# Kernel tuning notes

Measured on AMD Instinct MI355X. Metric: run time of the kernel, lower is better.

## Reference

```python
import jax, jax.numpy as jnp
import numpy as np

B, N, X_DIM, Y_DIM = 2048, 64, 2, 1
Z_DIM, R_DIM, H = 64, 128, 128
STEPS = 20
SIGMA_SQ = 1.0


def setup_inputs() -> dict:
    key = jax.random.key(0)
    ks = jax.random.split(key, 16)

    def w(k, shape):
        return jax.random.normal(k, shape, dtype=jnp.float32) / np.float32(np.sqrt(shape[0]))

    return {
        "x_ctx": jax.random.normal(ks[0], (B, N, X_DIM), jnp.float32),
        "y_ctx": jax.random.normal(ks[1], (B, N, Y_DIM), jnp.float32),
        "mask": jnp.ones((B, N, 1), jnp.float32),
        "z0": jax.random.normal(ks[2], (B, Z_DIM), jnp.float32),
        "noises": jax.random.normal(ks[3], (STEPS, B, Z_DIM), jnp.float32),
        "We1": w(ks[4], (X_DIM + Y_DIM, H)), "be1": jnp.zeros((H,), jnp.float32),
        "We2": w(ks[5], (H, H)), "be2": jnp.zeros((H,), jnp.float32),
        "We3": w(ks[6], (H, R_DIM)), "be3": jnp.zeros((R_DIM,), jnp.float32),
        "Wd1": w(ks[7], (Z_DIM + X_DIM, H)), "bd1": jnp.zeros((H,), jnp.float32),
        "Wd2": w(ks[8], (H, H)), "bd2": jnp.zeros((H,), jnp.float32),
        "Wd3": w(ks[9], (H, Y_DIM)), "bd3": jnp.zeros((Y_DIM,), jnp.float32),
        "Wf1": w(ks[10], (Z_DIM + R_DIM + 1, H)), "bf1": jnp.zeros((H,), jnp.float32),
        "Wf2": w(ks[11], (H, H)), "bf2": jnp.zeros((H,), jnp.float32),
        "Wf3": w(ks[12], (H, Z_DIM)), "bf3": jnp.zeros((Z_DIM,), jnp.float32),
        "steps": STEPS,
    }


def reference(x_ctx, y_ctx, mask, z0, noises,
              We1, be1, We2, be2, We3, be3,
              Wd1, bd1, Wd2, bd2, Wd3, bd3,
              Wf1, bf1, Wf2, bf2, Wf3, bf3,
              steps):
    silu = jax.nn.silu
    n_ctx = x_ctx.shape[1]

    # encoder: masked mean-pool set MLP -> r [B, R_DIM]
    h = silu(jnp.concatenate([x_ctx, y_ctx], axis=-1) @ We1 + be1)
    h = silu(h @ We2 + be2)
    h = h @ We3 + be3  # [B, N, R_DIM]
    r = jnp.sum(h * mask, axis=1) / jnp.clip(jnp.sum(mask, axis=1), 1e-6)

    def decoder(z):
        zb = jnp.broadcast_to(z[:, None, :], (z.shape[0], n_ctx, z.shape[1]))
        d = silu(jnp.concatenate([zb, x_ctx], axis=-1) @ Wd1 + bd1)
        d = silu(d @ Wd2 + bd2)
        return d @ Wd3 + bd3  # [B, N, Y_DIM]

    def energy_sum(z, t):
        # U_t(z) = u_prior + t * u_lik  (== (1-t)*u_prior + t*(u_prior + u_lik))
        u_prior = 0.5 * jnp.sum(z * z, axis=1)
        sq_err = (y_ctx - decoder(z)) ** 2 * mask
        u_lik = 0.5 * jnp.sum(sq_err, axis=(1, 2)) / SIGMA_SQ
        return jnp.sum(u_prior + t * u_lik)

    def drift(z, t_col):
        f = silu(jnp.concatenate([z, r, t_col], axis=-1) @ Wf1 + bf1)
        f = silu(f @ Wf2 + bf2)
        return f @ Wf3 + bf3

    dt = 1.0 / steps
    diff_coef = float(np.sqrt(2.0 * dt))

    def step(z, xs):
        t, noise = xs
        g = jnp.clip(jax.grad(energy_sum)(z, t), -100.0, 100.0)
        t_col = jnp.ones((z.shape[0], 1), z.dtype) * t
        b = drift(z, t_col)
        z = z + (-g + b) * dt + diff_coef * noise
        return z, None

    ts = jnp.arange(steps, dtype=jnp.float32) * dt
    z_final, _ = jax.lax.scan(jax.checkpoint(step), z0, (ts, noises))
    return z_final
```

## Files before the change

### kernel.cpp

```cpp
#include <hip/hip_runtime.h>
#include <math.h>


#define B_TOT 2048
#define NPT   64
#define ZD    64
#define HD    128

typedef short bh8 __attribute__((ext_vector_type(8)));
typedef float fx4 __attribute__((ext_vector_type(4)));

__device__ __forceinline__ float sigf(float x) {
  return __builtin_amdgcn_rcpf(1.0f + __expf(-x));
}
__device__ __forceinline__ unsigned int bfb(float x) {
  unsigned int u = __float_as_uint(x);
  u += 0x7FFFu + ((u >> 16) & 1u);
  return u >> 16;
}
__device__ __forceinline__ unsigned int cvtpk(float a, float b) {
  unsigned int r;
  asm("v_cvt_pk_bf16_f32 %0, %1, %2" : "=v"(r) : "v"(a), "v"(b));
  return r;
}
__device__ __forceinline__ float wsum64(float v) {
  #pragma unroll
  for (int d = 1; d < 64; d <<= 1) v += __shfl_xor(v, d, 64);
  return v;
}
__device__ __forceinline__ void wave_sync() {
  __builtin_amdgcn_wave_barrier();
  __builtin_amdgcn_s_waitcnt(0xC07F);
  __builtin_amdgcn_wave_barrier();
}

__global__ __launch_bounds__(256)
void prep_kernel(const float* __restrict__ Wd2, const float* __restrict__ We2,
                 const float* __restrict__ We3, const float* __restrict__ Wd1,
                 ushort* __restrict__ ws) {
  const int id = blockIdx.x * 256 + threadIdx.x;
  if (id < 65536) {
    const int arr = id >> 14;
    const int e = id & 16383;
    const int j = e & 7, L = (e >> 3) & 63, nt = (e >> 9) & 7, kc = e >> 12;
    const int kk = kc * 32 + (L >> 4) * 8 + j, nn = nt * 16 + (L & 15);
    float v;
    if      (arr == 0) v = Wd2[kk * HD + nn];
    else if (arr == 1) v = Wd2[nn * HD + kk];
    else if (arr == 2) v = We2[kk * HD + nn];
    else               v = We3[kk * HD + nn];
    ws[id] = (ushort)bfb(v);
  } else {
    const int e = id - 65536;
    const int h = e >> 6, jj = e & 63;
    ((float*)(ws + 65536))[e] = Wd1[jj * HD + h];
  }
}

__global__ __launch_bounds__(256, 4)
void metanets_kernel(
    const float* __restrict__ x_ctx, const float* __restrict__ y_ctx,
    const float* __restrict__ mask,  const float* __restrict__ z0,
    const float* __restrict__ noises,
    const float* __restrict__ We1, const float* __restrict__ be1,
    const float* __restrict__ be2, const float* __restrict__ be3,
    const float* __restrict__ Wd1, const float* __restrict__ bd1,
    const float* __restrict__ bd2, const float* __restrict__ Wd3,
    const float* __restrict__ bd3,
    const float* __restrict__ Wf1, const float* __restrict__ bf1,
    const float* __restrict__ Wf2, const float* __restrict__ bf2,
    const float* __restrict__ Wf3, const float* __restrict__ bf3,
    const ushort* __restrict__ wsfrag,
    float* __restrict__ out, int steps, float dt, float dco)
{
  __shared__ unsigned int h1f[4096];
  __shared__ float zsh[64];
  __shared__ float zw1[128];
  __shared__ float rsh[128];
  __shared__ float dsumP[512];
  __shared__ float dsumC[128];
  __shared__ float f1sh[128];
  __shared__ float f2sh[128];
  __shared__ float bgz[128];
  __shared__ float rw1sh[128];
  __shared__ float wt1sh[128];
  __shared__ float ysh[64], mksh[64];
  __shared__ float bd2sh[128], wd3sh[128], wx0sh[128], wx1sh[128];

  const int tid = threadIdx.x;
  const int lane = tid & 63;
  const int w = __builtin_amdgcn_readfirstlane(tid >> 6);
  const int b = blockIdx.x;
  const int rr = lane & 15, qq = lane >> 4;

  const bh8* Wd2f  = (const bh8*)(wsfrag);
  const bh8* Wd2Tf = (const bh8*)(wsfrag + 16384);
  const bh8* We2f  = (const bh8*)(wsfrag + 32768);
  const bh8* We3f  = (const bh8*)(wsfrag + 49152);
  const float* Wd1T = (const float*)(wsfrag + 65536);

  const float x0v = x_ctx[(b*NPT + lane)*2 + 0];
  const float x1v = x_ctx[(b*NPT + lane)*2 + 1];
  const float yv  = y_ctx[b*NPT + lane];
  const float mkv = mask[b*NPT + lane];
  const float inv_msum = 1.0f / fmaxf(wsum64(mkv), 1e-6f);
  const float bd3v = bd3[0];

  float x0q[4], x1q[4];
  #pragma unroll
  for (int g = 0; g < 4; ++g) {
    const int src = (w << 4) | (qq << 2) | g;
    x0q[g] = __shfl(x0v, src, 64);
    x1q[g] = __shfl(x1v, src, 64);
  }

  if (tid < 64) {
    zsh[tid]  = z0[b*ZD + tid];
    ysh[tid]  = yv;
    mksh[tid] = mkv;
  }
  if (tid < 128) {
    bd2sh[tid] = bd2[tid];
    wd3sh[tid] = Wd3[tid];
    wx0sh[tid] = Wd1[64*HD + tid];
    wx1sh[tid] = Wd1[65*HD + tid];
    f1sh[tid]  = be2[tid];
    f2sh[tid]  = be3[tid];
    wt1sh[tid] = Wf1[192*HD + tid];
  }
  __syncthreads();

  #pragma unroll
  for (int quad = 0; quad < 4; ++quad) {
    unsigned int pw[4];
    #pragma unroll
    for (int jj = 0; jj < 8; jj += 2) {
      const int k = 32*w + 8*quad + jj;
      const float sA = be1[k]   + x0v*We1[k]   + x1v*We1[HD+k]   + yv*We1[2*HD+k];
      const float sB = be1[k+1] + x0v*We1[k+1] + x1v*We1[HD+k+1] + yv*We1[2*HD+k+1];
      pw[jj>>1] = cvtpk(sA*sigf(sA), sB*sigf(sB));
    }
    uint4 v4; v4.x = pw[0]; v4.y = pw[1]; v4.z = pw[2]; v4.w = pw[3];
    ((uint4*)h1f)[(w*4 + (lane>>4))*64 + quad*16 + (lane&15)] = v4;
  }
  __syncthreads();

  {
    bh8 af[4];
    #pragma unroll
    for (int kc = 0; kc < 4; ++kc)
      af[kc] = ((const bh8*)h1f)[(kc*4 + w)*64 + lane];
    #pragma unroll 1
    for (int np = 0; np < 4; ++np) {
      const int nt0 = 2*np, nt1 = 2*np + 1;
      const bh8 a0 = We2f[(0*8+nt0)*64 + lane];
      const bh8 a1 = We2f[(1*8+nt0)*64 + lane];
      const bh8 a2 = We2f[(2*8+nt0)*64 + lane];
      const bh8 a3 = We2f[(3*8+nt0)*64 + lane];
      const bh8 c0 = We2f[(0*8+nt1)*64 + lane];
      const bh8 c1 = We2f[(1*8+nt1)*64 + lane];
      const bh8 c2 = We2f[(2*8+nt1)*64 + lane];
      const bh8 c3 = We2f[(3*8+nt1)*64 + lane];
      const float bv0 = f1sh[nt0*16 + rr], bv1 = f1sh[nt1*16 + rr];
      fx4 acc0 = (fx4){bv0, bv0, bv0, bv0};
      fx4 acc1 = (fx4){bv1, bv1, bv1, bv1};
      acc0 = __builtin_amdgcn_mfma_f32_16x16x32_bf16(af[0], a0, acc0, 0,0,0);
      acc1 = __builtin_amdgcn_mfma_f32_16x16x32_bf16(af[0], c0, acc1, 0,0,0);
      acc0 = __builtin_amdgcn_mfma_f32_16x16x32_bf16(af[1], a1, acc0, 0,0,0);
      acc1 = __builtin_amdgcn_mfma_f32_16x16x32_bf16(af[1], c1, acc1, 0,0,0);
      acc0 = __builtin_amdgcn_mfma_f32_16x16x32_bf16(af[2], a2, acc0, 0,0,0);
      acc1 = __builtin_amdgcn_mfma_f32_16x16x32_bf16(af[2], c2, acc1, 0,0,0);
      acc0 = __builtin_amdgcn_mfma_f32_16x16x32_bf16(af[3], a3, acc0, 0,0,0);
      acc1 = __builtin_amdgcn_mfma_f32_16x16x32_bf16(af[3], c3, acc1, 0,0,0);
      #pragma unroll
      for (int pi = 0; pi < 2; ++pi) {
        const int nt = pi ? nt1 : nt0;
        const fx4 acc = pi ? acc1 : acc0;
        #pragma unroll
        for (int g = 0; g < 4; ++g) {
          const float s2 = acc[g];
          const float tf = s2 * sigf(s2);
          const float pf = __shfl_xor(tf, 1, 64);
          if ((rr & 1) == 0) {
            const int unit = ((nt>>1)*4 + w)*64 + (2*(nt&1) + (rr>>3))*16 + 4*qq + g;
            h1f[unit*4 + ((rr&7)>>1)] = cvtpk(tf, pf);
          }
        }
      }
    }
  }
  wave_sync();

  {
    float mkq0, mkq1, mkq2, mkq3;
    {
      const int s0 = (w << 4) | (qq << 2);
      mkq0 = mksh[s0+0]; mkq1 = mksh[s0+1]; mkq2 = mksh[s0+2]; mkq3 = mksh[s0+3];
    }
    bh8 tf4[4];
    #pragma unroll
    for (int kc = 0; kc < 4; ++kc)
      tf4[kc] = ((const bh8*)h1f)[(kc*4 + w)*64 + lane];
    #pragma unroll 1
    for (int np = 0; np < 4; ++np) {
      const int nt0 = 2*np, nt1 = 2*np + 1;
      const bh8 a0 = We3f[(0*8+nt0)*64 + lane];
      const bh8 a1 = We3f[(1*8+nt0)*64 + lane];
      const bh8 a2 = We3f[(2*8+nt0)*64 + lane];
      const bh8 a3 = We3f[(3*8+nt0)*64 + lane];
      const bh8 c0 = We3f[(0*8+nt1)*64 + lane];
      const bh8 c1 = We3f[(1*8+nt1)*64 + lane];
      const bh8 c2 = We3f[(2*8+nt1)*64 + lane];
      const bh8 c3 = We3f[(3*8+nt1)*64 + lane];
      const float bv0 = f2sh[nt0*16 + rr], bv1 = f2sh[nt1*16 + rr];
      fx4 acc0 = (fx4){bv0, bv0, bv0, bv0};
      fx4 acc1 = (fx4){bv1, bv1, bv1, bv1};
      acc0 = __builtin_amdgcn_mfma_f32_16x16x32_bf16(tf4[0], a0, acc0, 0,0,0);
      acc1 = __builtin_amdgcn_mfma_f32_16x16x32_bf16(tf4[0], c0, acc1, 0,0,0);
      acc0 = __builtin_amdgcn_mfma_f32_16x16x32_bf16(tf4[1], a1, acc0, 0,0,0);
      acc1 = __builtin_amdgcn_mfma_f32_16x16x32_bf16(tf4[1], c1, acc1, 0,0,0);
      acc0 = __builtin_amdgcn_mfma_f32_16x16x32_bf16(tf4[2], a2, acc0, 0,0,0);
      acc1 = __builtin_amdgcn_mfma_f32_16x16x32_bf16(tf4[2], c2, acc1, 0,0,0);
      acc0 = __builtin_amdgcn_mfma_f32_16x16x32_bf16(tf4[3], a3, acc0, 0,0,0);
      acc1 = __builtin_amdgcn_mfma_f32_16x16x32_bf16(tf4[3], c3, acc1, 0,0,0);
      #pragma unroll
      for (int pi = 0; pi < 2; ++pi) {
        const int nt = pi ? nt1 : nt0;
        const fx4 acc = pi ? acc1 : acc0;
        float pv = mkq0*acc[0] + mkq1*acc[1] + mkq2*acc[2] + mkq3*acc[3];
        pv += __shfl_xor(pv, 16, 64);
        pv += __shfl_xor(pv, 32, 64);
        if (lane < 16) dsumP[w*128 + nt*16 + lane] = pv;
      }
    }
  }
  __syncthreads();
  if (tid < 128)
    rsh[tid] = (dsumP[tid] + dsumP[128+tid] + dsumP[256+tid] + dsumP[384+tid]) * inv_msum;
  __syncthreads();

  if (tid < 128) {
    float p0 = bf1[tid], p1 = 0.f, p2 = 0.f, p3 = 0.f;
    #pragma unroll 4
    for (int j = 0; j < 128; j += 4) {
      p0 = fmaf(rsh[j+0], Wf1[(64+j+0)*HD + tid], p0);
      p1 = fmaf(rsh[j+1], Wf1[(64+j+1)*HD + tid], p1);
      p2 = fmaf(rsh[j+2], Wf1[(64+j+2)*HD + tid], p2);
      p3 = fmaf(rsh[j+3], Wf1[(64+j+3)*HD + tid], p3);
    }
    rw1sh[tid] = (p0+p1) + (p2+p3);
  }
  __syncthreads();

  for (int st = 0; st < steps; ++st) {
    const float t = (float)st * dt;
    const int zi = tid & 63;

    const float noise_v = noises[(size_t)st * (B_TOT * ZD) + b * ZD + zi];
    const float zold_r  = zsh[zi];

    if (tid < 128) {
      float p0 = bd1[tid], p1 = 0.f, p2 = 0.f, p3 = 0.f;
      #pragma unroll 4
      for (int j = 0; j < 64; j += 4) {
        p0 = fmaf(zsh[j+0], Wd1[(j+0)*HD + tid], p0);
        p1 = fmaf(zsh[j+1], Wd1[(j+1)*HD + tid], p1);
        p2 = fmaf(zsh[j+2], Wd1[(j+2)*HD + tid], p2);
        p3 = fmaf(zsh[j+3], Wd1[(j+3)*HD + tid], p3);
      }
      zw1[tid] = (p0+p1) + (p2+p3);
    } else {
      const int o = tid - 128;
      float p0 = fmaf(t, wt1sh[o], rw1sh[o]);
      float p1 = 0.f, p2 = 0.f, p3 = 0.f;
      #pragma unroll 4
      for (int j = 0; j < 64; j += 4) {
        p0 = fmaf(zsh[j+0], Wf1[(j+0)*HD + o], p0);
        p1 = fmaf(zsh[j+1], Wf1[(j+1)*HD + o], p1);
        p2 = fmaf(zsh[j+2], Wf1[(j+2)*HD + o], p2);
        p3 = fmaf(zsh[j+3], Wf1[(j+3)*HD + o], p3);
      }
      const float a = (p0+p1) + (p2+p3);
      f1sh[o] = a * sigf(a);
    }
    __syncthreads();

    #pragma unroll
    for (int quad = 0; quad < 4; ++quad) {
      unsigned int pw[4];
      #pragma unroll
      for (int jj = 0; jj < 8; jj += 2) {
        const int k = 32*w + 8*quad + jj;
        const float sA = zw1[k]   + x0v*wx0sh[k]   + x1v*wx1sh[k];
        const float sB = zw1[k+1] + x0v*wx0sh[k+1] + x1v*wx1sh[k+1];
        pw[jj>>1] = cvtpk(sA*sigf(sA), sB*sigf(sB));
      }
      uint4 v4; v4.x = pw[0]; v4.y = pw[1]; v4.z = pw[2]; v4.w = pw[3];
      ((uint4*)h1f)[(w*4 + (lane>>4))*64 + quad*16 + (lane&15)] = v4;
    }
    __syncthreads();

    float ebw[4];
    {
      bh8 af[4];
      #pragma unroll
      for (int kc = 0; kc < 4; ++kc)
        af[kc] = ((const bh8*)h1f)[(kc*4 + w)*64 + lane];
      float da[4] = {0.f, 0.f, 0.f, 0.f};
      #pragma unroll 1
      for (int np = 0; np < 4; ++np) {
        const int nt0 = 2*np, nt1 = 2*np + 1;
        const bh8 a0 = Wd2f[(0*8+nt0)*64 + lane];
        const bh8 a1 = Wd2f[(1*8+nt0)*64 + lane];
        const bh8 a2 = Wd2f[(2*8+nt0)*64 + lane];
        const bh8 a3 = Wd2f[(3*8+nt0)*64 + lane];
        const bh8 c0 = Wd2f[(0*8+nt1)*64 + lane];
        const bh8 c1 = Wd2f[(1*8+nt1)*64 + lane];
        const bh8 c2 = Wd2f[(2*8+nt1)*64 + lane];
        const bh8 c3 = Wd2f[(3*8+nt1)*64 + lane];
        const float bv0 = bd2sh[nt0*16 + rr], bv1 = bd2sh[nt1*16 + rr];
        fx4 acc0 = (fx4){bv0, bv0, bv0, bv0};
        fx4 acc1 = (fx4){bv1, bv1, bv1, bv1};
        acc0 = __builtin_amdgcn_mfma_f32_16x16x32_bf16(af[0], a0, acc0, 0,0,0);
        acc1 = __builtin_amdgcn_mfma_f32_16x16x32_bf16(af[0], c0, acc1, 0,0,0);
        acc0 = __builtin_amdgcn_mfma_f32_16x16x32_bf16(af[1], a1, acc0, 0,0,0);
        acc1 = __builtin_amdgcn_mfma_f32_16x16x32_bf16(af[1], c1, acc1, 0,0,0);
        acc0 = __builtin_amdgcn_mfma_f32_16x16x32_bf16(af[2], a2, acc0, 0,0,0);
        acc1 = __builtin_amdgcn_mfma_f32_16x16x32_bf16(af[2], c2, acc1, 0,0,0);
        acc0 = __builtin_amdgcn_mfma_f32_16x16x32_bf16(af[3], a3, acc0, 0,0,0);
        acc1 = __builtin_amdgcn_mfma_f32_16x16x32_bf16(af[3], c3, acc1, 0,0,0);
        #pragma unroll
        for (int pi = 0; pi < 2; ++pi) {
          const int nt = pi ? nt1 : nt0;
          const fx4 acc = pi ? acc1 : acc0;
          const float w3 = wd3sh[nt*16 + rr];
          #pragma unroll
          for (int g = 0; g < 4; ++g) {
            const float s2 = acc[g];
            const float sg = sigf(s2);
            da[g] = fmaf(s2*sg, w3, da[g]);
            const float tf = w3 * (sg * fmaf(s2, 1.0f - sg, 1.0f));
            const float pf = __shfl_xor(tf, 1, 64);
            if ((rr & 1) == 0) {
              const int unit = ((nt>>1)*4 + w)*64 + (2*(nt&1) + (rr>>3))*16 + 4*qq + g;
              h1f[unit*4 + ((rr&7)>>1)] = cvtpk(tf, pf);
            }
          }
        }
      }
      const int s0 = (w << 4) | (qq << 2);
      #pragma unroll
      for (int g = 0; g < 4; ++g) {
        float v = da[g];
        v += __shfl_xor(v, 1, 64);
        v += __shfl_xor(v, 2, 64);
        v += __shfl_xor(v, 4, 64);
        v += __shfl_xor(v, 8, 64);
        ebw[g] = t * mksh[s0+g] * (v + bd3v - ysh[s0+g]);
      }
    }
    wave_sync();

    {
      bh8 tf4[4];
      #pragma unroll
      for (int kc = 0; kc < 4; ++kc)
        tf4[kc] = ((const bh8*)h1f)[(kc*4 + w)*64 + lane];
      #pragma unroll 1
      for (int np = 0; np < 4; ++np) {
        const int nt0 = 2*np, nt1 = 2*np + 1;
        const bh8 a0 = Wd2Tf[(0*8+nt0)*64 + lane];
        const bh8 a1 = Wd2Tf[(1*8+nt0)*64 + lane];
        const bh8 a2 = Wd2Tf[(2*8+nt0)*64 + lane];
        const bh8 a3 = Wd2Tf[(3*8+nt0)*64 + lane];
        const bh8 c0 = Wd2Tf[(0*8+nt1)*64 + lane];
        const bh8 c1 = Wd2Tf[(1*8+nt1)*64 + lane];
        const bh8 c2 = Wd2Tf[(2*8+nt1)*64 + lane];
        const bh8 c3 = Wd2Tf[(3*8+nt1)*64 + lane];
        fx4 u0 = (fx4){0.f, 0.f, 0.f, 0.f};
        fx4 u1 = (fx4){0.f, 0.f, 0.f, 0.f};
        u0 = __builtin_amdgcn_mfma_f32_16x16x32_bf16(tf4[0], a0, u0, 0,0,0);
        u1 = __builtin_amdgcn_mfma_f32_16x16x32_bf16(tf4[0], c0, u1, 0,0,0);
        u0 = __builtin_amdgcn_mfma_f32_16x16x32_bf16(tf4[1], a1, u0, 0,0,0);
        u1 = __builtin_amdgcn_mfma_f32_16x16x32_bf16(tf4[1], c1, u1, 0,0,0);
        u0 = __builtin_amdgcn_mfma_f32_16x16x32_bf16(tf4[2], a2, u0, 0,0,0);
        u1 = __builtin_amdgcn_mfma_f32_16x16x32_bf16(tf4[2], c2, u1, 0,0,0);
        u0 = __builtin_amdgcn_mfma_f32_16x16x32_bf16(tf4[3], a3, u0, 0,0,0);
        u1 = __builtin_amdgcn_mfma_f32_16x16x32_bf16(tf4[3], c3, u1, 0,0,0);
        #pragma unroll
        for (int pi = 0; pi < 2; ++pi) {
          const int nt = pi ? nt1 : nt0;
          const fx4 u = pi ? u1 : u0;
          const float zv = zw1[nt*16 + rr];
          const float wa = wx0sh[nt*16 + rr];
          const float wb = wx1sh[nt*16 + rr];
          float snt = 0.f;
          #pragma unroll
          for (int g = 0; g < 4; ++g) {
            const float s1 = zv + x0q[g]*wa + x1q[g]*wb;
            const float sg = sigf(s1);
            snt += ebw[g] * (sg * fmaf(s1, 1.0f - sg, 1.0f)) * u[g];
          }
          snt += __shfl_xor(snt, 16, 64);
          snt += __shfl_xor(snt, 32, 64);
          if (lane < 16) dsumP[w*128 + nt*16 + lane] = snt;
        }
      }
    }
    __syncthreads();

    if (tid < 128) {
      dsumC[tid] = dsumP[tid] + dsumP[128+tid] + dsumP[256+tid] + dsumP[384+tid];
      float p0 = 0.f, p1 = 0.f, p2 = 0.f, p3 = 0.f;
      #pragma unroll 4
      for (int j = 64; j < 128; j += 4) {
        p0 = fmaf(f1sh[j+0], Wf2[(j+0)*HD + tid], p0);
        p1 = fmaf(f1sh[j+1], Wf2[(j+1)*HD + tid], p1);
        p2 = fmaf(f1sh[j+2], Wf2[(j+2)*HD + tid], p2);
        p3 = fmaf(f1sh[j+3], Wf2[(j+3)*HD + tid], p3);
      }
      rsh[tid] = (p0+p1) + (p2+p3);
    } else {
      const int o = tid - 128;
      float p0 = bf2[o], p1 = 0.f, p2 = 0.f, p3 = 0.f;
      #pragma unroll 4
      for (int j = 0; j < 64; j += 4) {
        p0 = fmaf(f1sh[j+0], Wf2[(j+0)*HD + o], p0);
        p1 = fmaf(f1sh[j+1], Wf2[(j+1)*HD + o], p1);
        p2 = fmaf(f1sh[j+2], Wf2[(j+2)*HD + o], p2);
        p3 = fmaf(f1sh[j+3], Wf2[(j+3)*HD + o], p3);
      }
      zw1[o] = (p0+p1) + (p2+p3);
    }
    __syncthreads();

    if (tid < 128) {
      const int j = tid & 63, h0 = (tid >> 6) * 64;
      float p0 = 0.f, p1 = 0.f, p2 = 0.f, p3 = 0.f;
      #pragma unroll 4
      for (int h = 0; h < 64; h += 4) {
        p0 = fmaf(dsumC[h0+h+0], Wd1T[(h0+h+0)*64 + j], p0);
        p1 = fmaf(dsumC[h0+h+1], Wd1T[(h0+h+1)*64 + j], p1);
        p2 = fmaf(dsumC[h0+h+2], Wd1T[(h0+h+2)*64 + j], p2);
        p3 = fmaf(dsumC[h0+h+3], Wd1T[(h0+h+3)*64 + j], p3);
      }
      dsumP[tid] = (p0+p1) + (p2+p3);
    } else {
      const int o = tid - 128;
      const float a = rsh[o] + zw1[o];
      f2sh[o] = a * sigf(a);
      wave_sync();
      const int j = o & 63, h0 = (o >> 6) * 64;
      float p0 = (h0 == 0) ? bf3[j] : 0.f;
      float p1 = 0.f, p2 = 0.f, p3 = 0.f;
      #pragma unroll 4
      for (int h = 0; h < 64; h += 4) {
        p0 = fmaf(f2sh[h0+h+0], Wf3[(h0+h+0)*ZD + j], p0);
        p1 = fmaf(f2sh[h0+h+1], Wf3[(h0+h+1)*ZD + j], p1);
        p2 = fmaf(f2sh[h0+h+2], Wf3[(h0+h+2)*ZD + j], p2);
        p3 = fmaf(f2sh[h0+h+3], Wf3[(h0+h+3)*ZD + j], p3);
      }
      bgz[o] = (p0+p1) + (p2+p3);
    }
    __syncthreads();

    {
      const float bdrift = bgz[zi] + bgz[64 + zi];
      const float gzv    = dsumP[zi] + dsumP[64 + zi];
      float g = zold_r + gzv;
      g = fminf(fmaxf(g, -100.0f), 100.0f);
      zsh[zi] = zold_r + (bdrift - g) * dt + dco * noise_v;
    }
    wave_sync();
  }

  if (tid < 64) out[b * ZD + tid] = zsh[tid];
}

extern "C" void kernel_launch(void* const* d_in, const int* in_sizes, int n_in,
                              void* d_out, int out_size, void* d_ws, size_t ws_size,
                              hipStream_t stream) {
  const float* x_ctx  = (const float*)d_in[0];
  const float* y_ctx  = (const float*)d_in[1];
  const float* mask   = (const float*)d_in[2];
  const float* z0     = (const float*)d_in[3];
  const float* noises = (const float*)d_in[4];
  const float* We1 = (const float*)d_in[5];  const float* be1 = (const float*)d_in[6];
  const float* We2 = (const float*)d_in[7];  const float* be2 = (const float*)d_in[8];
  const float* We3 = (const float*)d_in[9];  const float* be3 = (const float*)d_in[10];
  const float* Wd1 = (const float*)d_in[11]; const float* bd1 = (const float*)d_in[12];
  const float* Wd2 = (const float*)d_in[13]; const float* bd2 = (const float*)d_in[14];
  const float* Wd3 = (const float*)d_in[15]; const float* bd3 = (const float*)d_in[16];
  const float* Wf1 = (const float*)d_in[17]; const float* bf1 = (const float*)d_in[18];
  const float* Wf2 = (const float*)d_in[19]; const float* bf2 = (const float*)d_in[20];
  const float* Wf3 = (const float*)d_in[21]; const float* bf3 = (const float*)d_in[22];

  const int steps = in_sizes[4] / (B_TOT * ZD);
  const float dt  = 1.0f / (float)steps;
  const float dco = (float)sqrt(2.0 / (double)steps);

  ushort* wsu = (ushort*)d_ws;

  hipLaunchKernelGGL(prep_kernel, dim3(288), dim3(256), 0, stream,
                     Wd2, We2, We3, Wd1, wsu);
  hipLaunchKernelGGL(metanets_kernel, dim3(B_TOT), dim3(256), 0, stream,
      x_ctx, y_ctx, mask, z0, noises,
      We1, be1, be2, be3,
      Wd1, bd1, bd2, Wd3, bd3,
      Wf1, bf1, Wf2, bf2, Wf3, bf3,
      wsu, (float*)d_out, steps, dt, dco);
}
```

Before: 838.0 us.

## Use packed fp32 FMA with pair-interleaved weight layouts for small GEMVs

Prep kernel now writes Wd1, Wf1, Wf2, Wf3 and transposed Wd1 into pair-interleaved fp32 layouts so each thread loads a float2 and issues a packed FMA. The first-layer GEMV is remapped so every wave computes half decoder and half drift outputs, and its block barrier becomes a wave barrier. This aims to halve FMA instruction count and widen loads in the per-step small matvecs. The wave-local sync depends on each wave consuming only the zw1/f1sh entries it wrote, and the interleaved layout adds workspace and prep cost.

```diff
diff --git a/kernel.cpp b/kernel.cpp
--- a/kernel.cpp
+++ b/kernel.cpp
@@ -9,6 +9,7 @@
 
 typedef short bh8 __attribute__((ext_vector_type(8)));
 typedef float fx4 __attribute__((ext_vector_type(4)));
+typedef float fx2 __attribute__((ext_vector_type(2)));
 
 __device__ __forceinline__ float sigf(float x) {
   return __builtin_amdgcn_rcpf(1.0f + __expf(-x));
@@ -23,6 +24,9 @@
   asm("v_cvt_pk_bf16_f32 %0, %1, %2" : "=v"(r) : "v"(a), "v"(b));
   return r;
 }
+__device__ __forceinline__ fx2 pkfma(fx2 a, fx2 b, fx2 c) {
+  return __builtin_elementwise_fma(a, b, c);
+}
 __device__ __forceinline__ float wsum64(float v) {
   #pragma unroll
   for (int d = 1; d < 64; d <<= 1) v += __shfl_xor(v, d, 64);
@@ -37,7 +41,8 @@
 __global__ __launch_bounds__(256)
 void prep_kernel(const float* __restrict__ Wd2, const float* __restrict__ We2,
                  const float* __restrict__ We3, const float* __restrict__ Wd1,
-                 ushort* __restrict__ ws) {
+                 const float* __restrict__ Wf1, const float* __restrict__ Wf2,
+                 const float* __restrict__ Wf3, ushort* __restrict__ ws) {
   const int id = blockIdx.x * 256 + threadIdx.x;
   if (id < 65536) {
     const int arr = id >> 14;
@@ -50,10 +55,26 @@
     else if (arr == 2) v = We2[kk * HD + nn];
     else               v = We3[kk * HD + nn];
     ws[id] = (ushort)bfb(v);
+  } else if (id < 73728) {
+    const int e = id - 65536;
+    const int j2 = e >> 8, o = (e >> 1) & 127, lohi = e & 1;
+    ((float*)(ws + 65536))[e] = Wd1[(2*j2 + lohi)*HD + o];
+  } else if (id < 81920) {
+    const int e = id - 73728;
+    const int j2 = e >> 8, o = (e >> 1) & 127, lohi = e & 1;
+    ((float*)(ws + 81920))[e] = Wf1[(2*j2 + lohi)*HD + o];
+  } else if (id < 98304) {
+    const int e = id - 81920;
+    const int j2 = e >> 8, o = (e >> 1) & 127, lohi = e & 1;
+    ((float*)(ws + 98304))[e] = Wf2[(2*j2 + lohi)*HD + o];
+  } else if (id < 106496) {
+    const int e = id - 98304;
+    const int h2 = e >> 7, j = (e >> 1) & 63, lohi = e & 1;
+    ((float*)(ws + 131072))[e] = Wf3[(2*h2 + lohi)*ZD + j];
   } else {
-    const int e = id - 65536;
-    const int h = e >> 6, jj = e & 63;
-    ((float*)(ws + 65536))[e] = Wd1[jj * HD + h];
+    const int e = id - 106496;
+    const int h2 = e >> 7, j = (e >> 1) & 63, lohi = e & 1;
+    ((float*)(ws + 147456))[e] = Wd1[j*HD + (2*h2 + lohi)];
   }
 }
 
@@ -74,13 +95,13 @@
     float* __restrict__ out, int steps, float dt, float dco)
 {
   __shared__ unsigned int h1f[4096];
-  __shared__ float zsh[64];
-  __shared__ float zw1[128];
+  __shared__ __align__(8) float zsh[64];
+  __shared__ __align__(8) float zw1[128];
   __shared__ float rsh[128];
+  __shared__ __align__(8) float dsumC[128];
   __shared__ float dsumP[512];
-  __shared__ float dsumC[128];
-  __shared__ float f1sh[128];
-  __shared__ float f2sh[128];
+  __shared__ __align__(8) float f1sh[128];
+  __shared__ __align__(8) float f2sh[128];
   __shared__ float bgz[128];
   __shared__ float rw1sh[128];
   __shared__ float wt1sh[128];
@@ -97,7 +118,11 @@
   const bh8* Wd2Tf = (const bh8*)(wsfrag + 16384);
   const bh8* We2f  = (const bh8*)(wsfrag + 32768);
   const bh8* We3f  = (const bh8*)(wsfrag + 49152);
-  const float* Wd1T = (const float*)(wsfrag + 65536);
+  const fx2* Wd1P  = (const fx2*)(wsfrag + 65536);
+  const fx2* Wf1zP = (const fx2*)(wsfrag + 81920);
+  const fx2* Wf2P  = (const fx2*)(wsfrag + 98304);
+  const fx2* Wf3P  = (const fx2*)(wsfrag + 131072);
+  const fx2* Wd1TP = (const fx2*)(wsfrag + 147456);
 
   const float x0v = x_ctx[(b*NPT + lane)*2 + 0];
   const float x1v = x_ctx[(b*NPT + lane)*2 + 1];
@@ -259,31 +284,28 @@
     const float noise_v = noises[(size_t)st * (B_TOT * ZD) + b * ZD + zi];
     const float zold_r  = zsh[zi];
 
-    if (tid < 128) {
-      float p0 = bd1[tid], p1 = 0.f, p2 = 0.f, p3 = 0.f;
+    {
+      const int oA = 32*w + (lane & 31);
+      const bool isz = (lane < 32);
+      const fx2* Wp = (isz ? Wd1P : Wf1zP) + oA;
+      fx2 a0 = (fx2){ isz ? bd1[oA] : fmaf(t, wt1sh[oA], rw1sh[oA]), 0.f };
+      fx2 a1 = (fx2){0.f, 0.f}, a2 = a1, a3 = a1;
       #pragma unroll 4
-      for (int j = 0; j < 64; j += 4) {
-        p0 = fmaf(zsh[j+0], Wd1[(j+0)*HD + tid], p0);
-        p1 = fmaf(zsh[j+1], Wd1[(j+1)*HD + tid], p1);
-        p2 = fmaf(zsh[j+2], Wd1[(j+2)*HD + tid], p2);
-        p3 = fmaf(zsh[j+3], Wd1[(j+3)*HD + tid], p3);
-      }
-      zw1[tid] = (p0+p1) + (p2+p3);
-    } else {
-      const int o = tid - 128;
-      float p0 = fmaf(t, wt1sh[o], rw1sh[o]);
-      float p1 = 0.f, p2 = 0.f, p3 = 0.f;
-      #pragma unroll 4
-      for (int j = 0; j < 64; j += 4) {
-        p0 = fmaf(zsh[j+0], Wf1[(j+0)*HD + o], p0);
-        p1 = fmaf(zsh[j+1], Wf1[(j+1)*HD + o], p1);
-        p2 = fmaf(zsh[j+2], Wf1[(j+2)*HD + o], p2);
-        p3 = fmaf(zsh[j+3], Wf1[(j+3)*HD + o], p3);
-      }
-      const float a = (p0+p1) + (p2+p3);
-      f1sh[o] = a * sigf(a);
-    }
-    __syncthreads();
+      for (int j2 = 0; j2 < 32; j2 += 4) {
+        const fx2 z0 = *(const fx2*)&zsh[2*(j2+0)];
+        const fx2 z1 = *(const fx2*)&zsh[2*(j2+1)];
+        const fx2 z2 = *(const fx2*)&zsh[2*(j2+2)];
+        const fx2 z3 = *(const fx2*)&zsh[2*(j2+3)];
+        a0 = pkfma(z0, Wp[(j2+0)*128], a0);
+        a1 = pkfma(z1, Wp[(j2+1)*128], a1);
+        a2 = pkfma(z2, Wp[(j2+2)*128], a2);
+        a3 = pkfma(z3, Wp[(j2+3)*128], a3);
+      }
+      const float a = ((a0.x+a0.y)+(a1.x+a1.y)) + ((a2.x+a2.y)+(a3.x+a3.y));
+      if (isz) zw1[oA] = a;
+      else     f1sh[oA] = a * sigf(a);
+    }
+    wave_sync();
 
     #pragma unroll
     for (int quad = 0; quad < 4; ++quad) {
@@ -411,56 +433,76 @@
 
     if (tid < 128) {
       dsumC[tid] = dsumP[tid] + dsumP[128+tid] + dsumP[256+tid] + dsumP[384+tid];
-      float p0 = 0.f, p1 = 0.f, p2 = 0.f, p3 = 0.f;
+      const fx2* Wp = Wf2P + tid;
+      fx2 a0 = (fx2){0.f, 0.f}, a1 = a0, a2 = a0, a3 = a0;
       #pragma unroll 4
-      for (int j = 64; j < 128; j += 4) {
-        p0 = fmaf(f1sh[j+0], Wf2[(j+0)*HD + tid], p0);
-        p1 = fmaf(f1sh[j+1], Wf2[(j+1)*HD + tid], p1);
-        p2 = fmaf(f1sh[j+2], Wf2[(j+2)*HD + tid], p2);
-        p3 = fmaf(f1sh[j+3], Wf2[(j+3)*HD + tid], p3);
-      }
-      rsh[tid] = (p0+p1) + (p2+p3);
+      for (int j2 = 32; j2 < 64; j2 += 4) {
+        const fx2 f0 = *(const fx2*)&f1sh[2*(j2+0)];
+        const fx2 f1v = *(const fx2*)&f1sh[2*(j2+1)];
+        const fx2 f2v = *(const fx2*)&f1sh[2*(j2+2)];
+        const fx2 f3v = *(const fx2*)&f1sh[2*(j2+3)];
+        a0 = pkfma(f0,  Wp[(j2+0)*128], a0);
+        a1 = pkfma(f1v, Wp[(j2+1)*128], a1);
+        a2 = pkfma(f2v, Wp[(j2+2)*128], a2);
+        a3 = pkfma(f3v, Wp[(j2+3)*128], a3);
+      }
+      rsh[tid] = ((a0.x+a0.y)+(a1.x+a1.y)) + ((a2.x+a2.y)+(a3.x+a3.y));
     } else {
       const int o = tid - 128;
-      float p0 = bf2[o], p1 = 0.f, p2 = 0.f, p3 = 0.f;
+      const fx2* Wp = Wf2P + o;
+      fx2 a0 = (fx2){bf2[o], 0.f}, a1 = (fx2){0.f,0.f}, a2 = a1, a3 = a1;
       #pragma unroll 4
-      for (int j = 0; j < 64; j += 4) {
-        p0 = fmaf(f1sh[j+0], Wf2[(j+0)*HD + o], p0);
-        p1 = fmaf(f1sh[j+1], Wf2[(j+1)*HD + o], p1);
-        p2 = fmaf(f1sh[j+2], Wf2[(j+2)*HD + o], p2);
-        p3 = fmaf(f1sh[j+3], Wf2[(j+3)*HD + o], p3);
-      }
-      zw1[o] = (p0+p1) + (p2+p3);
+      for (int j2 = 0; j2 < 32; j2 += 4) {
+        const fx2 f0 = *(const fx2*)&f1sh[2*(j2+0)];
+        const fx2 f1v = *(const fx2*)&f1sh[2*(j2+1)];
+        const fx2 f2v = *(const fx2*)&f1sh[2*(j2+2)];
+        const fx2 f3v = *(const fx2*)&f1sh[2*(j2+3)];
+        a0 = pkfma(f0,  Wp[(j2+0)*128], a0);
+        a1 = pkfma(f1v, Wp[(j2+1)*128], a1);
+        a2 = pkfma(f2v, Wp[(j2+2)*128], a2);
+        a3 = pkfma(f3v, Wp[(j2+3)*128], a3);
+      }
+      zw1[o] = ((a0.x+a0.y)+(a1.x+a1.y)) + ((a2.x+a2.y)+(a3.x+a3.y));
     }
     __syncthreads();
 
     if (tid < 128) {
-      const int j = tid & 63, h0 = (tid >> 6) * 64;
-      float p0 = 0.f, p1 = 0.f, p2 = 0.f, p3 = 0.f;
+      const int j = tid & 63, h2b = (tid >> 6) * 32;
+      const fx2* Wp = Wd1TP + j;
+      fx2 a0 = (fx2){0.f, 0.f}, a1 = a0, a2 = a0, a3 = a0;
       #pragma unroll 4
-      for (int h = 0; h < 64; h += 4) {
-        p0 = fmaf(dsumC[h0+h+0], Wd1T[(h0+h+0)*64 + j], p0);
-        p1 = fmaf(dsumC[h0+h+1], Wd1T[(h0+h+1)*64 + j], p1);
-        p2 = fmaf(dsumC[h0+h+2], Wd1T[(h0+h+2)*64 + j], p2);
-        p3 = fmaf(dsumC[h0+h+3], Wd1T[(h0+h+3)*64 + j], p3);
-      }
-      dsumP[tid] = (p0+p1) + (p2+p3);
+      for (int h2 = 0; h2 < 32; h2 += 4) {
+        const fx2 d0 = *(const fx2*)&dsumC[2*(h2b+h2+0)];
+        const fx2 d1 = *(const fx2*)&dsumC[2*(h2b+h2+1)];
+        const fx2 d2 = *(const fx2*)&dsumC[2*(h2b+h2+2)];
+        const fx2 d3 = *(const fx2*)&dsumC[2*(h2b+h2+3)];
+        a0 = pkfma(d0, Wp[(h2b+h2+0)*64], a0);
+        a1 = pkfma(d1, Wp[(h2b+h2+1)*64], a1);
+        a2 = pkfma(d2, Wp[(h2b+h2+2)*64], a2);
+        a3 = pkfma(d3, Wp[(h2b+h2+3)*64], a3);
+      }
+      dsumP[tid] = ((a0.x+a0.y)+(a1.x+a1.y)) + ((a2.x+a2.y)+(a3.x+a3.y));
     } else {
       const int o = tid - 128;
-      const float a = rsh[o] + zw1[o];
-      f2sh[o] = a * sigf(a);
+      const float aa = rsh[o] + zw1[o];
+      f2sh[o] = aa * sigf(aa);
       wave_sync();
-      const int j = o & 63, h0 = (o >> 6) * 64;
-      float p0 = (h0 == 0) ? bf3[j] : 0.f;
-      float p1 = 0.f, p2 = 0.f, p3 = 0.f;
+      const int j = o & 63, h2b = (o >> 6) * 32;
+      const fx2* Wp = Wf3P + j;
+      fx2 a0 = (fx2){ (h2b == 0) ? bf3[j] : 0.f, 0.f };
+      fx2 a1 = (fx2){0.f, 0.f}, a2 = a1, a3 = a1;
       #pragma unroll 4
-      for (int h = 0; h < 64; h += 4) {
-        p0 = fmaf(f2sh[h0+h+0], Wf3[(h0+h+0)*ZD + j], p0);
-        p1 = fmaf(f2sh[h0+h+1], Wf3[(h0+h+1)*ZD + j], p1);
-        p2 = fmaf(f2sh[h0+h+2], Wf3[(h0+h+2)*ZD + j], p2);
-        p3 = fmaf(f2sh[h0+h+3], Wf3[(h0+h+3)*ZD + j], p3);
-      }
-      bgz[o] = (p0+p1) + (p2+p3);
+      for (int h2 = 0; h2 < 32; h2 += 4) {
+        const fx2 f0 = *(const fx2*)&f2sh[2*(h2b+h2+0)];
+        const fx2 f1v = *(const fx2*)&f2sh[2*(h2b+h2+1)];
+        const fx2 f2v = *(const fx2*)&f2sh[2*(h2b+h2+2)];
+        const fx2 f3v = *(const fx2*)&f2sh[2*(h2b+h2+3)];
+        a0 = pkfma(f0,  Wp[(h2b+h2+0)*64], a0);
+        a1 = pkfma(f1v, Wp[(h2b+h2+1)*64], a1);
+        a2 = pkfma(f2v, Wp[(h2b+h2+2)*64], a2);
+        a3 = pkfma(f3v, Wp[(h2b+h2+3)*64], a3);
+      }
+      bgz[o] = ((a0.x+a0.y)+(a1.x+a1.y)) + ((a2.x+a2.y)+(a3.x+a3.y));
     }
     __syncthreads();
 
@@ -501,8 +543,8 @@
 
   ushort* wsu = (ushort*)d_ws;
 
-  hipLaunchKernelGGL(prep_kernel, dim3(288), dim3(256), 0, stream,
-                     Wd2, We2, We3, Wd1, wsu);
+  hipLaunchKernelGGL(prep_kernel, dim3(448), dim3(256), 0, stream,
+                     Wd2, We2, We3, Wd1, Wf1, Wf2, Wf3, wsu);
   hipLaunchKernelGGL(metanets_kernel, dim3(B_TOT), dim3(256), 0, stream,
       x_ctx, y_ctx, mask, z0, noises,
       We1, be1, be2, be3,
```

New measurement: 1.093 ms. +30.4%, slower.
